# Kernel optimization log

Hardware: AMD Instinct MI355X
Metric: run time of the kernel (lower is better)

The kernel has to match this reference:

```python
import jax, jax.numpy as jnp
import numpy as np

B, L, D, H = 2, 2048, 1024, 16
DH = D // H            # head depth = 64
LEN_CONTEXT = 2048 + 1 # module stores len_context + 1


def setup_inputs() -> dict:
    key = jax.random.key(0)
    ks = jax.random.split(key, 9)
    s = 0.02
    return {
        "query": jax.random.normal(ks[0], (B, L, D), jnp.float32),
        "key":   jax.random.normal(ks[1], (B, L, D), jnp.float32),
        "value": jax.random.normal(ks[2], (B, L, D), jnp.float32),
        "Wq": jax.random.normal(ks[3], (D, D), jnp.float32) * s,
        "bq": jnp.zeros((D,), jnp.float32),
        "Wk": jax.random.normal(ks[4], (D, D), jnp.float32) * s,
        "bk": jnp.zeros((D,), jnp.float32),
        "Wv": jax.random.normal(ks[5], (D, D), jnp.float32) * s,
        "bv": jnp.zeros((D,), jnp.float32),
        "Wo": jax.random.normal(ks[6], (D, D), jnp.float32) * s,
        "bo": jnp.zeros((D,), jnp.float32),
        "rel": jax.random.normal(ks[7], (LEN_CONTEXT, DH), jnp.float32) * s,
    }


def _split_heads(x):
    # [B, L, D] -> [B, H, L, DH]
    return x.reshape(B, L, H, DH).transpose(0, 2, 1, 3)


def reference(query, key, value, Wq, bq, Wk, bk, Wv, bv, Wo, bo, rel):
    q = _split_heads(query @ Wq + bq)   # [B,H,L,DH]
    k = _split_heads(key @ Wk + bk)
    v = _split_heads(value @ Wv + bv)

    # relative embedding slice: rel[max(0, len_context - len_q):]
    start = max(0, LEN_CONTEXT - L)
    e = rel[start:, :]                  # [M, DH], M = L here
    M = e.shape[0]

    qe = jnp.einsum('bhld,md->bhlm', q, e)  # [B,H,L,M]

    # _qe_masking: keep qe[l, m] where m >= M-1-l (upper anti-triangle)
    mask = (jnp.arange(M)[None, :] >= (M - 1 - jnp.arange(L))[:, None]).astype(qe.dtype)
    qe = qe * mask

    # _skewing: pad 1 on left of last dim, reshape swapping last two dims, drop first row
    padded = jnp.pad(qe, ((0, 0), (0, 0), (0, 0), (1, 0)))        # [B,H,L,M+1]
    reshaped = padded.reshape(B, H, M + 1, L)
    srel = reshaped[:, :, 1:, :]                                  # [B,H,L,L] (len_k == len_q)

    logits = (jnp.einsum('bhld,bhmd->bhlm', q, k) + srel) / jnp.sqrt(jnp.float32(DH))
    # NOTE: the original code builds a directional mask but never adds it to logits
    attn = jax.nn.softmax(logits, axis=-1)
    out = jnp.einsum('bhlm,bhmd->bhld', attn, v)                  # [B,H,L,DH]
    out = out.transpose(0, 2, 1, 3).reshape(B, L, D)
    return out @ Wo + bo
```

## Files before the change

### kernel.cpp

```cpp
#include <hip/hip_runtime.h>
#include <hip/hip_bf16.h>


typedef __bf16 v8bf __attribute__((ext_vector_type(8)));
typedef __bf16 v4bf __attribute__((ext_vector_type(4)));
typedef float f32x4 __attribute__((ext_vector_type(4)));
typedef float f32x16 __attribute__((ext_vector_type(16)));

#define MFMA16(A,B,C) __builtin_amdgcn_mfma_f32_16x16x32_bf16((A),(B),(C),0,0,0)
#define MFMA32(A,B,C) __builtin_amdgcn_mfma_f32_32x32x16_bf16((A),(B),(C),0,0,0)

constexpr float kQScale = 0.1803368801111244f;

__global__ __launch_bounds__(256)
void cast_rel(const float* __restrict__ rel, __bf16* __restrict__ E)
{
    const int i = blockIdx.x * 256 + threadIdx.x;
    if (i >= 2304 * 16) return;
    const int base = i * 4;
    const int row = base >> 6;
    const int prow = row - 128;
    v4bf o;
    if (prow >= 0 && prow < 2048) {
        const float4 v = *reinterpret_cast<const float4*>(&rel[(size_t)(prow + 1) * 64 + (base & 63)]);
        o[0] = (__bf16)v.x; o[1] = (__bf16)v.y; o[2] = (__bf16)v.z; o[3] = (__bf16)v.w;
    } else {
        o[0] = (__bf16)0.f; o[1] = (__bf16)0.f; o[2] = (__bf16)0.f; o[3] = (__bf16)0.f;
    }
    *reinterpret_cast<v4bf*>(&E[base]) = o;
}

__global__ __launch_bounds__(256)
void transpose_cast_w4(const float* __restrict__ W0, const float* __restrict__ W1,
                       const float* __restrict__ W2, const float* __restrict__ W3,
                       __bf16* __restrict__ Wt4)
{
    __shared__ float tile[64][65];
    const int z = blockIdx.z;
    const float* W = (z == 0) ? W0 : (z == 1) ? W1 : (z == 2) ? W2 : W3;
    __bf16* Wt = Wt4 + (size_t)z * 1048576;
    const int r0 = blockIdx.y * 64, c0 = blockIdx.x * 64;
    const int tr = threadIdx.x >> 4;
    const int tc = (threadIdx.x & 15) * 4;
    #pragma unroll
    for (int p = 0; p < 4; ++p) {
        const int r = tr + p * 16;
        const float4 v = *reinterpret_cast<const float4*>(&W[(size_t)(r0 + r) * 1024 + c0 + tc]);
        tile[r][tc + 0] = v.x; tile[r][tc + 1] = v.y; tile[r][tc + 2] = v.z; tile[r][tc + 3] = v.w;
    }
    __syncthreads();
    #pragma unroll
    for (int p = 0; p < 4; ++p) {
        const int cr = tr + p * 16;
        v4bf o;
        o[0] = (__bf16)tile[tc + 0][cr];
        o[1] = (__bf16)tile[tc + 1][cr];
        o[2] = (__bf16)tile[tc + 2][cr];
        o[3] = (__bf16)tile[tc + 3][cr];
        *reinterpret_cast<v4bf*>(&Wt[(size_t)(c0 + cr) * 1024 + r0 + tc]) = o;
    }
}

template <bool ABF16>
__device__ __forceinline__
void gemm_body(const float* __restrict__ Af, const __bf16* __restrict__ Ab,
               const __bf16* __restrict__ Wt, const float* __restrict__ bias,
               float* __restrict__ Cf, __bf16* __restrict__ Cb, int mode,
               float oscale, int bx, int by)
{
    __shared__ __bf16 As[2][128 * 64];
    __shared__ __bf16 Ws[2][128 * 64];
    const int tid = threadIdx.x;
    const int wid = tid >> 6, lane = tid & 63, g = lane >> 4, li = lane & 15;
    const int r0 = by * 128, c0 = bx * 128;
    const int wr = wid >> 1, wc = wid & 1;
    const int sr = tid >> 3, sb = tid & 7;

    f32x4 acc[4][4];
    #pragma unroll
    for (int a = 0; a < 4; ++a)
        #pragma unroll
        for (int b2 = 0; b2 < 4; ++b2) acc[a][b2] = f32x4{0.f, 0.f, 0.f, 0.f};

    v8bf areg[4], wreg[4];

    auto loadA = [&](int p, int kt) -> v8bf {
        if constexpr (ABF16) {
            return *reinterpret_cast<const v8bf*>(&Ab[(size_t)(r0 + sr + 32 * p) * 1024 + kt + sb * 8]);
        } else {
            const float* ar = &Af[(size_t)(r0 + sr + 32 * p) * 1024 + kt + sb * 8];
            const float4 f0 = *reinterpret_cast<const float4*>(ar);
            const float4 f1 = *reinterpret_cast<const float4*>(ar + 4);
            v8bf a8;
            a8[0] = (__bf16)f0.x; a8[1] = (__bf16)f0.y; a8[2] = (__bf16)f0.z; a8[3] = (__bf16)f0.w;
            a8[4] = (__bf16)f1.x; a8[5] = (__bf16)f1.y; a8[6] = (__bf16)f1.z; a8[7] = (__bf16)f1.w;
            return a8;
        }
    };
    auto loadW = [&](int p, int kt) -> v8bf {
        return *reinterpret_cast<const v8bf*>(&Wt[(size_t)(c0 + sr + 32 * p) * 1024 + kt + sb * 8]);
    };

    #pragma unroll
    for (int p = 0; p < 4; ++p) { areg[p] = loadA(p, 0); wreg[p] = loadW(p, 0); }
    #pragma unroll
    for (int p = 0; p < 4; ++p) {
        const int row = sr + 32 * p;
        *reinterpret_cast<v8bf*>(&As[0][row * 64 + ((sb ^ (row & 7)) << 3)]) = areg[p];
        *reinterpret_cast<v8bf*>(&Ws[0][row * 64 + ((sb ^ (row & 7)) << 3)]) = wreg[p];
    }
    __syncthreads();

    for (int ki = 0; ki < 16; ++ki) {
        const int cur = ki & 1;
        if (ki < 15) {
            const int kt = (ki + 1) * 64;
            #pragma unroll
            for (int p = 0; p < 4; ++p) { areg[p] = loadA(p, kt); wreg[p] = loadW(p, kt); }
        }
        #pragma unroll
        for (int ks = 0; ks < 2; ++ks) {
            v8bf af[4], bfr[4];
            #pragma unroll
            for (int fm = 0; fm < 4; ++fm) {
                const int row = wr * 64 + fm * 16 + li;
                af[fm] = *reinterpret_cast<const v8bf*>(
                    &As[cur][row * 64 + (((ks * 4 + g) ^ (row & 7)) << 3)]);
            }
            #pragma unroll
            for (int fn = 0; fn < 4; ++fn) {
                const int row = wc * 64 + fn * 16 + li;
                bfr[fn] = *reinterpret_cast<const v8bf*>(
                    &Ws[cur][row * 64 + (((ks * 4 + g) ^ (row & 7)) << 3)]);
            }
            __builtin_amdgcn_s_setprio(1);
            #pragma unroll
            for (int fm = 0; fm < 4; ++fm)
                #pragma unroll
                for (int fn = 0; fn < 4; ++fn)
                    acc[fm][fn] = MFMA16(af[fm], bfr[fn], acc[fm][fn]);
            __builtin_amdgcn_s_setprio(0);
        }
        if (ki < 15) {
            const int nxt = cur ^ 1;
            #pragma unroll
            for (int p = 0; p < 4; ++p) {
                const int row = sr + 32 * p;
                *reinterpret_cast<v8bf*>(&As[nxt][row * 64 + ((sb ^ (row & 7)) << 3)]) = areg[p];
                *reinterpret_cast<v8bf*>(&Ws[nxt][row * 64 + ((sb ^ (row & 7)) << 3)]) = wreg[p];
            }
        }
        __syncthreads();
    }

    #pragma unroll
    for (int fn = 0; fn < 4; ++fn) {
        const int col = c0 + wc * 64 + fn * 16 + li;
        const float bb = bias[col];
        #pragma unroll
        for (int fm = 0; fm < 4; ++fm) {
            if (mode == 2) {
                const int row = r0 + wr * 64 + fm * 16 + 4 * g;
                const int b = row >> 11, l = row & 2047;
                const int h = col >> 6, dh = col & 63;
                v4bf pk;
                #pragma unroll
                for (int reg = 0; reg < 4; ++reg)
                    pk[reg] = (__bf16)(acc[fm][fn][reg] + bb);
                *reinterpret_cast<v4bf*>(&Cb[((size_t)((b * 16 + h) * 64 + dh)) * 2048 + l]) = pk;
            } else {
                #pragma unroll
                for (int reg = 0; reg < 4; ++reg) {
                    const int row = r0 + wr * 64 + fm * 16 + 4 * g + reg;
                    const float val = acc[fm][fn][reg] + bb;
                    if (mode == 0) {
                        Cf[(size_t)row * 1024 + col] = val;
                    } else {
                        const int b = row >> 11, l = row & 2047, h = col >> 6, dh = col & 63;
                        Cb[((size_t)(b * 16 + h) * 2048 + l) * 64 + dh] = (__bf16)(val * oscale);
                    }
                }
            }
        }
    }
}

__global__ __launch_bounds__(256)
void gemm_proj3(const float* __restrict__ Aq, const float* __restrict__ Ak,
                const float* __restrict__ Av, const __bf16* __restrict__ Wt4,
                const float* __restrict__ bq, const float* __restrict__ bk,
                const float* __restrict__ bv, __bf16* __restrict__ qo,
                __bf16* __restrict__ ko, __bf16* __restrict__ vto)
{
    const int z = blockIdx.z;
    const float* A = (z == 0) ? Aq : (z == 1) ? Ak : Av;
    const __bf16* Wt = Wt4 + (size_t)z * 1048576;
    const float* bias = (z == 0) ? bq : (z == 1) ? bk : bv;
    __bf16* Cb = (z == 0) ? qo : (z == 1) ? ko : vto;
    const float osc = (z == 0) ? kQScale : 1.0f;
    gemm_body<false>(A, nullptr, Wt, bias, nullptr, Cb, (z == 2) ? 2 : 1, osc,
                     blockIdx.x, blockIdx.y);
}

__global__ __launch_bounds__(256)
void gemm_out(const __bf16* __restrict__ A, const __bf16* __restrict__ Wt,
              const float* __restrict__ bias, float* __restrict__ C)
{
    gemm_body<true>(nullptr, A, Wt, bias, C, nullptr, 0, 1.0f, blockIdx.x, blockIdx.y);
}

__global__ __launch_bounds__(256, 2)
void attn_mfma(const __bf16* __restrict__ q, const __bf16* __restrict__ k,
               const __bf16* __restrict__ vt, const __bf16* __restrict__ Ep,
               __bf16* __restrict__ ao)
{
    __shared__ __bf16 Kl[64 * 64];
    __shared__ __bf16 Vl[64 * 64];
    __shared__ __bf16 Tl[4][32 * 132];
    __shared__ __bf16 Pl[4][32 * 72];

    const int tid = threadIdx.x;
    const int wid = tid >> 6;
    const int lane = tid & 63;
    const int l31 = lane & 31;
    const int g2 = lane >> 5;

    const int flat = blockIdx.y * 16 + blockIdx.x;
    const int jj_ = flat >> 3;
    const int bh = (flat & 7) * 4 + (jj_ >> 4);
    const int qt = jj_ & 15;

    const int l0 = qt * 128;
    const int lw0 = l0 + wid * 32;
    const size_t hbase = (size_t)bh * (2048 * 64);
    const __bf16* qp = q + hbase;
    const __bf16* kp = k + hbase;
    const __bf16* vtp = vt + hbase;
    const int wb0 = 1984 - l0 - 32 * wid;

    __bf16* Tw = &Tl[wid][0];
    __bf16* Pw = &Pl[wid][0];

    v8bf qf[4];
    {
        const __bf16* qrow = qp + (size_t)(lw0 + l31) * 64 + g2 * 8;
        qf[0] = *reinterpret_cast<const v8bf*>(qrow);
        qf[1] = *reinterpret_cast<const v8bf*>(qrow + 16);
        qf[2] = *reinterpret_cast<const v8bf*>(qrow + 32);
        qf[3] = *reinterpret_cast<const v8bf*>(qrow + 48);
    }

    const int sr = tid >> 3, sb = tid & 7;

    auto eload = [&](int baseRow, v8bf eb[8]) {
        #pragma unroll
        for (int jc = 0; jc < 2; ++jc)
            #pragma unroll
            for (int ks = 0; ks < 4; ++ks)
                eb[jc * 4 + ks] = *reinterpret_cast<const v8bf*>(
                    Ep + (long)(baseRow + jc * 32 + l31) * 64 + ks * 16 + g2 * 8);
    };

    auto tgemm = [&](const v8bf eb[8], int colBase) {
        #pragma unroll
        for (int jc = 0; jc < 2; ++jc) {
            f32x16 tacc;
            #pragma unroll
            for (int r = 0; r < 16; ++r) tacc[r] = 0.f;
            __builtin_amdgcn_s_setprio(1);
            #pragma unroll
            for (int ks = 0; ks < 4; ++ks)
                tacc = MFMA32(eb[jc * 4 + ks], qf[ks], tacc);
            __builtin_amdgcn_s_setprio(0);
            #pragma unroll
            for (int r2 = 0; r2 < 4; ++r2) {
                v4bf w;
                w[0] = (__bf16)tacc[4 * r2 + 0]; w[1] = (__bf16)tacc[4 * r2 + 1];
                w[2] = (__bf16)tacc[4 * r2 + 2]; w[3] = (__bf16)tacc[4 * r2 + 3];
                const int col = colBase + jc * 32 + 8 * r2 + 4 * g2;
                *reinterpret_cast<v4bf*>(Tw + l31 * 132 + col) = w;
            }
        }
    };

    {
        const v8bf k0a = *reinterpret_cast<const v8bf*>(kp + (size_t)sr * 64 + sb * 8);
        const v8bf k0b = *reinterpret_cast<const v8bf*>(kp + (size_t)(sr + 32) * 64 + sb * 8);
        const v8bf v0a = *reinterpret_cast<const v8bf*>(vtp + (size_t)sr * 2048 + sb * 8);
        const v8bf v0b = *reinterpret_cast<const v8bf*>(vtp + (size_t)(sr + 32) * 2048 + sb * 8);
        v8bf ebA[8], ebB[8];
        eload(wb0, ebA);
        eload(wb0 + 64, ebB);
        *reinterpret_cast<v8bf*>(&Kl[sr * 64 + ((sb ^ (sr & 7)) << 3)]) = k0a;
        *reinterpret_cast<v8bf*>(&Kl[(sr + 32) * 64 + ((sb ^ (sr & 7)) << 3)]) = k0b;
        *reinterpret_cast<v8bf*>(&Vl[sr * 64 + ((sb ^ (sr & 7)) << 3)]) = v0a;
        *reinterpret_cast<v8bf*>(&Vl[(sr + 32) * 64 + ((sb ^ (sr & 7)) << 3)]) = v0b;
        __syncthreads();
        tgemm(ebA, 0);
        tgemm(ebB, 64);
    }

    f32x16 oacc[2];
    #pragma unroll
    for (int dc = 0; dc < 2; ++dc)
        #pragma unroll
        for (int r = 0; r < 16; ++r) oacc[dc][r] = 0.f;
    float lrow = 0.f;

    for (int t = 0; t < 32; ++t) {
        const int m0 = t * 64;
        const bool lastT = (t == 31);
        const bool needRel = (m0 <= lw0 + 31);
        const bool fullAdd = (m0 + 63 <= lw0);
        const bool needTnext = (m0 + 64 <= lw0 + 31);
        const int lob = 64 * (t & 1);

        v8bf ebN[8];
        if (needTnext) eload(wb0 + 64 * t + 128, ebN);

        v8bf kra, krb, vra, vrb;
        if (!lastT) {
            const int m1 = m0 + 64;
            kra = *reinterpret_cast<const v8bf*>(kp + (size_t)(m1 + sr) * 64 + sb * 8);
            krb = *reinterpret_cast<const v8bf*>(kp + (size_t)(m1 + sr + 32) * 64 + sb * 8);
            vra = *reinterpret_cast<const v8bf*>(vtp + (size_t)sr * 2048 + m1 + sb * 8);
            vrb = *reinterpret_cast<const v8bf*>(vtp + (size_t)(sr + 32) * 2048 + m1 + sb * 8);
        }

        #pragma unroll
        for (int mc = 0; mc < 2; ++mc) {
            f32x16 sacc;
            #pragma unroll
            for (int r = 0; r < 16; ++r) sacc[r] = 0.f;
            __builtin_amdgcn_s_setprio(1);
            #pragma unroll
            for (int ks = 0; ks < 4; ++ks) {
                const int row = mc * 32 + l31;
                const v8bf kb = *reinterpret_cast<const v8bf*>(
                    &Kl[row * 64 + (((2 * ks + g2) ^ (l31 & 7)) << 3)]);
                sacc = MFMA32(kb, qf[ks], sacc);
            }
            __builtin_amdgcn_s_setprio(0);

            if (needRel) {
                const int cb = 63 - l31 + lob;
                if (fullAdd) {
                    #pragma unroll
                    for (int r2 = 0; r2 < 4; ++r2)
                        #pragma unroll
                        for (int i2 = 0; i2 < 4; ++i2) {
                            const int mtl = mc * 32 + 8 * r2 + 4 * g2 + i2;
                            const int c = (cb + mtl) & 127;
                            sacc[4 * r2 + i2] += (float)Tw[l31 * 132 + c];
                        }
                } else {
                    const int R = lw0 + l31 - m0;
                    #pragma unroll
                    for (int r2 = 0; r2 < 4; ++r2)
                        #pragma unroll
                        for (int i2 = 0; i2 < 4; ++i2) {
                            const int mtl = mc * 32 + 8 * r2 + 4 * g2 + i2;
                            const int c = (cb + mtl) & 127;
                            const float tv = (float)Tw[l31 * 132 + c];
                            sacc[4 * r2 + i2] += (mtl <= R) ? tv : 0.f;
                        }
                }
            }

            #pragma unroll
            for (int jj = 0; jj < 4; ++jj) {
                const float p0 = exp2f(sacc[4 * jj + 0]);
                const float p1 = exp2f(sacc[4 * jj + 1]);
                const float p2 = exp2f(sacc[4 * jj + 2]);
                const float p3 = exp2f(sacc[4 * jj + 3]);
                lrow += (p0 + p1) + (p2 + p3);
                v4bf w;
                w[0] = (__bf16)p0; w[1] = (__bf16)p1; w[2] = (__bf16)p2; w[3] = (__bf16)p3;
                *reinterpret_cast<v4bf*>(Pw + l31 * 72 + mc * 32 + 8 * jj + 4 * g2) = w;
            }
        }

        if (needTnext) tgemm(ebN, lob);

        #pragma unroll
        for (int ks = 0; ks < 4; ++ks) {
            const v8bf pa = *reinterpret_cast<const v8bf*>(Pw + l31 * 72 + ks * 16 + g2 * 8);
            __builtin_amdgcn_s_setprio(1);
            #pragma unroll
            for (int dc = 0; dc < 2; ++dc) {
                const int row = dc * 32 + l31;
                const v8bf vb = *reinterpret_cast<const v8bf*>(
                    &Vl[row * 64 + (((2 * ks + g2) ^ (l31 & 7)) << 3)]);
                oacc[dc] = MFMA32(vb, pa, oacc[dc]);
            }
            __builtin_amdgcn_s_setprio(0);
        }

        __syncthreads();
        if (!lastT) {
            *reinterpret_cast<v8bf*>(&Kl[sr * 64 + ((sb ^ (sr & 7)) << 3)]) = kra;
            *reinterpret_cast<v8bf*>(&Kl[(sr + 32) * 64 + ((sb ^ (sr & 7)) << 3)]) = krb;
            *reinterpret_cast<v8bf*>(&Vl[sr * 64 + ((sb ^ (sr & 7)) << 3)]) = vra;
            *reinterpret_cast<v8bf*>(&Vl[(sr + 32) * 64 + ((sb ^ (sr & 7)) << 3)]) = vrb;
        }
        __syncthreads();
    }

    lrow += __shfl_xor(lrow, 32);
    const float inv = 1.0f / lrow;

    __syncthreads();
    __bf16* Ol = &Tl[0][0];
    #pragma unroll
    for (int dc = 0; dc < 2; ++dc)
        #pragma unroll
        for (int r2 = 0; r2 < 4; ++r2) {
            v4bf w;
            w[0] = (__bf16)(oacc[dc][4 * r2 + 0] * inv);
            w[1] = (__bf16)(oacc[dc][4 * r2 + 1] * inv);
            w[2] = (__bf16)(oacc[dc][4 * r2 + 2] * inv);
            w[3] = (__bf16)(oacc[dc][4 * r2 + 3] * inv);
            const int d0 = dc * 32 + 8 * r2 + 4 * g2;
            *reinterpret_cast<v4bf*>(Ol + (wid * 32 + l31) * 72 + d0) = w;
        }
    __syncthreads();

    const int b = bh >> 4, h = bh & 15;
    #pragma unroll
    for (int p = 0; p < 4; ++p) {
        const int row = p * 32 + (tid >> 3);
        const v8bf w = *reinterpret_cast<const v8bf*>(Ol + row * 72 + (tid & 7) * 8);
        *reinterpret_cast<v8bf*>(ao + (size_t)(b * 2048 + l0 + row) * 1024 + h * 64 + (tid & 7) * 8) = w;
    }
}

extern "C" void kernel_launch(void* const* d_in, const int* in_sizes, int n_in,
                              void* d_out, int out_size, void* d_ws, size_t ws_size,
                              hipStream_t stream) {
    (void)in_sizes; (void)n_in; (void)out_size; (void)ws_size;
    const float* query = (const float*)d_in[0];
    const float* key   = (const float*)d_in[1];
    const float* value = (const float*)d_in[2];
    const float* Wq    = (const float*)d_in[3];
    const float* bq    = (const float*)d_in[4];
    const float* Wk    = (const float*)d_in[5];
    const float* bk    = (const float*)d_in[6];
    const float* Wv    = (const float*)d_in[7];
    const float* bv    = (const float*)d_in[8];
    const float* Wo    = (const float*)d_in[9];
    const float* bo    = (const float*)d_in[10];
    const float* rel   = (const float*)d_in[11];
    float* out = (float*)d_out;

    __bf16* q_bf  = (__bf16*)d_ws;
    __bf16* k_bf  = q_bf + 4194304;
    __bf16* vt_bf = k_bf + 4194304;
    __bf16* Wt4   = vt_bf + 4194304;
    __bf16* E_pad = Wt4 + 4194304;
    __bf16* aob   = E_pad + 147456;

    const dim3 blk(256);

    cast_rel<<<144, blk, 0, stream>>>(rel, E_pad);
    transpose_cast_w4<<<dim3(16, 16, 4), blk, 0, stream>>>(Wq, Wk, Wv, Wo, Wt4);
    gemm_proj3<<<dim3(8, 32, 3), blk, 0, stream>>>(query, key, value, Wt4,
                                                   bq, bk, bv, q_bf, k_bf, vt_bf);
    attn_mfma<<<dim3(16, 32), blk, 0, stream>>>(q_bf, k_bf, vt_bf,
                                                E_pad + 128 * 64, aob);
    gemm_out<<<dim3(8, 32), blk, 0, stream>>>(aob, Wt4 + 3 * 1048576, bo, out);
}
```

Baseline: 205.2 us.

## Swizzle attention LDS tiles with XOR and remap GEMM blocks across XCDs

The padded per-wave T and P shared-memory tiles (row strides 132 and 72) become unpadded tiles (strides 128 and 64) with an XOR swizzle on the column index, shrinking LDS use and changing the bank-conflict pattern. The projection and output GEMM kernels also remap their block indices so that blocks dispatched round-robin to the same XCD work on neighbouring tiles, which should improve L2 reuse of A and weight tiles. The swizzle adds a few integer ops per access, and the remap assumes an 8x32 grid shape.

```diff
diff --git a/kernel.cpp b/kernel.cpp
--- a/kernel.cpp
+++ b/kernel.cpp
@@ -185,6 +185,15 @@
     }
 }
 
+__device__ __forceinline__ void xcd_remap_gemm(int& bx, int& by)
+{
+    const int flat = by * 8 + bx;
+    const int xcd = flat & 7;
+    const int idx = flat >> 3;
+    by = xcd * 4 + (idx & 3);
+    bx = idx >> 2;
+}
+
 __global__ __launch_bounds__(256)
 void gemm_proj3(const float* __restrict__ Aq, const float* __restrict__ Ak,
                 const float* __restrict__ Av, const __bf16* __restrict__ Wt4,
@@ -198,15 +207,18 @@
     const float* bias = (z == 0) ? bq : (z == 1) ? bk : bv;
     __bf16* Cb = (z == 0) ? qo : (z == 1) ? ko : vto;
     const float osc = (z == 0) ? kQScale : 1.0f;
-    gemm_body<false>(A, nullptr, Wt, bias, nullptr, Cb, (z == 2) ? 2 : 1, osc,
-                     blockIdx.x, blockIdx.y);
+    int bx = blockIdx.x, by = blockIdx.y;
+    xcd_remap_gemm(bx, by);
+    gemm_body<false>(A, nullptr, Wt, bias, nullptr, Cb, (z == 2) ? 2 : 1, osc, bx, by);
 }
 
 __global__ __launch_bounds__(256)
 void gemm_out(const __bf16* __restrict__ A, const __bf16* __restrict__ Wt,
               const float* __restrict__ bias, float* __restrict__ C)
 {
-    gemm_body<true>(nullptr, A, Wt, bias, C, nullptr, 0, 1.0f, blockIdx.x, blockIdx.y);
+    int bx = blockIdx.x, by = blockIdx.y;
+    xcd_remap_gemm(bx, by);
+    gemm_body<true>(nullptr, A, Wt, bias, C, nullptr, 0, 1.0f, bx, by);
 }
 
 __global__ __launch_bounds__(256, 2)
@@ -216,14 +228,15 @@
 {
     __shared__ __bf16 Kl[64 * 64];
     __shared__ __bf16 Vl[64 * 64];
-    __shared__ __bf16 Tl[4][32 * 132];
-    __shared__ __bf16 Pl[4][32 * 72];
+    __shared__ __bf16 Tl[4][32 * 128];
+    __shared__ __bf16 Pl[4][32 * 64];
 
     const int tid = threadIdx.x;
     const int wid = tid >> 6;
     const int lane = tid & 63;
     const int l31 = lane & 31;
     const int g2 = lane >> 5;
+    const int xsh = (l31 & 7) << 3;
 
     const int flat = blockIdx.y * 16 + blockIdx.x;
     const int jj_ = flat >> 3;
@@ -278,7 +291,7 @@
                 w[0] = (__bf16)tacc[4 * r2 + 0]; w[1] = (__bf16)tacc[4 * r2 + 1];
                 w[2] = (__bf16)tacc[4 * r2 + 2]; w[3] = (__bf16)tacc[4 * r2 + 3];
                 const int col = colBase + jc * 32 + 8 * r2 + 4 * g2;
-                *reinterpret_cast<v4bf*>(Tw + l31 * 132 + col) = w;
+                *reinterpret_cast<v4bf*>(Tw + l31 * 128 + (col ^ xsh)) = w;
             }
         }
     };
@@ -351,7 +364,7 @@
                         for (int i2 = 0; i2 < 4; ++i2) {
                             const int mtl = mc * 32 + 8 * r2 + 4 * g2 + i2;
                             const int c = (cb + mtl) & 127;
-                            sacc[4 * r2 + i2] += (float)Tw[l31 * 132 + c];
+                            sacc[4 * r2 + i2] += (float)Tw[l31 * 128 + (c ^ xsh)];
                         }
                 } else {
                     const int R = lw0 + l31 - m0;
@@ -361,7 +374,7 @@
                         for (int i2 = 0; i2 < 4; ++i2) {
                             const int mtl = mc * 32 + 8 * r2 + 4 * g2 + i2;
                             const int c = (cb + mtl) & 127;
-                            const float tv = (float)Tw[l31 * 132 + c];
+                            const float tv = (float)Tw[l31 * 128 + (c ^ xsh)];
                             sacc[4 * r2 + i2] += (mtl <= R) ? tv : 0.f;
                         }
                 }
@@ -376,7 +389,8 @@
                 lrow += (p0 + p1) + (p2 + p3);
                 v4bf w;
                 w[0] = (__bf16)p0; w[1] = (__bf16)p1; w[2] = (__bf16)p2; w[3] = (__bf16)p3;
-                *reinterpret_cast<v4bf*>(Pw + l31 * 72 + mc * 32 + 8 * jj + 4 * g2) = w;
+                const int col = mc * 32 + 8 * jj + 4 * g2;
+                *reinterpret_cast<v4bf*>(Pw + l31 * 64 + (col ^ xsh)) = w;
             }
         }
 
@@ -384,7 +398,8 @@
 
         #pragma unroll
         for (int ks = 0; ks < 4; ++ks) {
-            const v8bf pa = *reinterpret_cast<const v8bf*>(Pw + l31 * 72 + ks * 16 + g2 * 8);
+            const v8bf pa = *reinterpret_cast<const v8bf*>(
+                Pw + l31 * 64 + ((ks * 16 + g2 * 8) ^ xsh));
             __builtin_amdgcn_s_setprio(1);
             #pragma unroll
             for (int dc = 0; dc < 2; ++dc) {
```

New measurement: 187.0 us. -8.9%, faster.
